# Kernel tuning notes

Measured on AMD Instinct MI355X. Metric: run time of the kernel, lower is better.

The kernel has to match this reference:

```python
import jax, jax.numpy as jnp
import numpy as np

D_MODEL = 1024
N_HEAD = 16
D_K = 64
D_V = 64
D_INNER = 4096
MAX_REL = 16
EPS = 1e-6


def _rel_index(length_q, length_k):
    # Shaw-style clipped relative distance matrix -> indices into embedding table
    dist = jnp.arange(length_k)[None, :] - jnp.arange(length_q)[:, None]
    return jnp.clip(dist, -MAX_REL, MAX_REL) + MAX_REL  # [Lq, Lk] in [0, 2*MAX_REL]


def _layer_norm(x, gamma, beta):
    mu = jnp.mean(x, axis=-1, keepdims=True)
    var = jnp.var(x, axis=-1, keepdims=True)
    return (x - mu) / jnp.sqrt(var + EPS) * gamma + beta


def setup_inputs() -> dict:
    key = jax.random.key(0)
    ks = jax.random.split(key, 16)
    B, L = 8, 1024
    s = 0.02
    inp = {
        "q": jax.random.normal(ks[0], (B, L, D_MODEL), jnp.float32),
        "k": jax.random.normal(ks[1], (B, L, D_MODEL), jnp.float32),
        "v": jax.random.normal(ks[2], (B, L, D_MODEL), jnp.float32),
        "wq": jax.random.normal(ks[3], (D_MODEL, D_MODEL), jnp.float32) * s,
        "bq": jnp.zeros((D_MODEL,), jnp.float32),
        "wk": jax.random.normal(ks[4], (D_MODEL, D_MODEL), jnp.float32) * s,
        "bk": jnp.zeros((D_MODEL,), jnp.float32),
        "wv": jax.random.normal(ks[5], (D_MODEL, D_MODEL), jnp.float32) * s,
        "bv": jnp.zeros((D_MODEL,), jnp.float32),
        "wfc": jax.random.normal(ks[6], (D_MODEL, D_MODEL), jnp.float32) * s,
        "bfc": jnp.zeros((D_MODEL,), jnp.float32),
        "w1": jax.random.normal(ks[7], (D_MODEL, D_INNER), jnp.float32) * s,
        "b1": jnp.zeros((D_INNER,), jnp.float32),
        "w2": jax.random.normal(ks[8], (D_INNER, D_MODEL), jnp.float32) * s,
        "b2": jnp.zeros((D_MODEL,), jnp.float32),
        "ln_g": jnp.ones((D_MODEL,), jnp.float32),
        "ln_b": jnp.zeros((D_MODEL,), jnp.float32),
        "rel_k": jax.random.normal(ks[9], (2 * MAX_REL + 1, D_K), jnp.float32) * s,
        "rel_v": jax.random.normal(ks[10], (2 * MAX_REL + 1, D_V), jnp.float32) * s,
    }
    return inp


def reference(q, k, v, wq, bq, wk, bk, wv, bv, wfc, bfc, w1, b1, w2, b2, ln_g, ln_b, rel_k, rel_v):
    B, Lq, _ = q.shape
    Lk = k.shape[1]
    residual = q

    Q = q @ wq + bq  # [B, Lq, D]
    K = k @ wk + bk
    V = v @ wv + bv

    Qh = Q.reshape(B, Lq, N_HEAD, D_K)  # [B, Lq, H, dk]
    Kh = K.reshape(B, Lk, N_HEAD, D_K)
    Vh = V.reshape(B, Lk, N_HEAD, D_V)

    # content-content scores
    attn1 = jnp.einsum("bqhd,bkhd->bhqk", Qh, Kh)
    # content-position scores (Shaw relative position)
    idx = _rel_index(Lq, Lk)  # [Lq, Lk]
    k2 = rel_k[idx]           # [Lq, Lk, dk]
    attn2 = jnp.einsum("bqhd,qkd->bhqk", Qh, k2)

    attn = (attn1 + attn2) / jnp.sqrt(jnp.float32(D_K))
    attn = jax.nn.softmax(attn, axis=-1)  # dropout = identity (eval)

    weight1 = jnp.einsum("bhqk,bkhd->bhqd", attn, Vh)
    v2 = rel_v[idx]  # [Lq, Lk, dv]
    weight2 = jnp.einsum("bhqk,qkd->bhqd", attn, v2)

    out = (weight1 + weight2).transpose(0, 2, 1, 3).reshape(B, Lq, N_HEAD * D_V)
    out = out @ wfc + bfc
    out = out + residual
    out = _layer_norm(out, ln_g, ln_b)

    residual = out
    out2 = jax.nn.relu(out @ w1 + b1) @ w2 + b2
    out = _layer_norm(out2 + residual, ln_g, ln_b)  # same LN params reused, as in source
    return out
```

## Files before the change

kernel.cpp:

```cpp
#include <hip/hip_runtime.h>
#include <stdint.h>


typedef __bf16 bf16x8 __attribute__((ext_vector_type(8)));
typedef float  f32x4  __attribute__((ext_vector_type(4)));

__device__ __forceinline__ unsigned short f2bf(float f) {
  __bf16 h = (__bf16)f;
  union { __bf16 h; unsigned short u; } x; x.h = h;
  return x.u;
}

__device__ __forceinline__ void gload_lds16(
    const unsigned short* g,
    __attribute__((address_space(3))) unsigned int* l) {
  __builtin_amdgcn_global_load_lds(
      (const __attribute__((address_space(1))) unsigned int*)g, l, 16, 0, 0);
}

template<int EPI>
__global__ __launch_bounds__(512, 2) void gemm_bt(
    const unsigned short* __restrict__ A,
    const unsigned short* __restrict__ Bt,
    const float* __restrict__ bias0,
    const float* __restrict__ bias1,
    const float* __restrict__ bias2,
    void* __restrict__ Cout,
    int M, int N, int K,
    size_t sA, size_t sB, size_t sC)
{
  __shared__ __align__(16) unsigned short S[3 * 24576];
  const int tid = threadIdx.x;
  const int lane = tid & 63, wv = tid >> 6;
  const int lq = lane >> 4, lm = lane & 15;
  const int wr = wv >> 2, wc = wv & 3;

  const int z = blockIdx.z;
  const float* bias = (z == 0) ? bias0 : (z == 1) ? bias1 : bias2;
  A  += (size_t)z * sA;
  Bt += (size_t)z * sB;

  const int nx = gridDim.x;
  const int nwg = nx * gridDim.y;
  int bid = blockIdx.y * nx + blockIdx.x;
  bid = (bid & 7) * (nwg >> 3) + (bid >> 3);
  const int m0 = (bid / nx) * 256, n0 = (bid % nx) * 128;

  const int srow = tid >> 3;
  const int scol = ((tid & 7) ^ (srow & 7)) * 8;
  const unsigned short* ga = A  + (size_t)(m0 + srow) * K + scol;
  const unsigned short* gb = Bt + (size_t)(n0 + srow) * K + scol;

  __attribute__((address_space(3))) unsigned int* lbase =
      (__attribute__((address_space(3))) unsigned int*)S;

  f32x4 acc[8][2] = {};

  auto stage = [&](int buf) {
    __attribute__((address_space(3))) unsigned int* lA = lbase + buf * 12288 + wv * 256;
    __attribute__((address_space(3))) unsigned int* lB = lA + 8192;
    #pragma unroll
    for (int g = 0; g < 4; ++g)
      gload_lds16(ga + (size_t)(g * 64) * K, lA + g * 2048);
    #pragma unroll
    for (int g = 0; g < 2; ++g)
      gload_lds16(gb + (size_t)(g * 64) * K, lB + g * 2048);
    ga += 64; gb += 64;
  };

  const int csw0 = ((lq ^ (lm & 7)) << 4);
  const int csw1 = csw0 ^ 64;
  const char* fa = (const char*)S + (wr * 128 + lm) * 128;
  const char* fb = (const char*)S + 32768 + (wc * 32 + lm) * 128;

  auto compute_tile = [&](int buf) {
    const char* ba = fa + buf * 49152;
    const char* bb = fb + buf * 49152;
    bf16x8 bfr[2][2];
    #pragma unroll
    for (int j = 0; j < 2; ++j) {
      bfr[j][0] = *(const bf16x8*)(bb + j * 2048 + csw0);
      bfr[j][1] = *(const bf16x8*)(bb + j * 2048 + csw1);
    }
    #pragma unroll
    for (int q = 0; q < 4; ++q) {
      bf16x8 af[2][2];
      #pragma unroll
      for (int ii = 0; ii < 2; ++ii) {
        af[ii][0] = *(const bf16x8*)(ba + (q * 2 + ii) * 2048 + csw0);
        af[ii][1] = *(const bf16x8*)(ba + (q * 2 + ii) * 2048 + csw1);
      }
      __builtin_amdgcn_s_barrier();
      __builtin_amdgcn_s_setprio(1);
      #pragma unroll
      for (int ii = 0; ii < 2; ++ii)
        #pragma unroll
        for (int j = 0; j < 2; ++j)
          #pragma unroll
          for (int kk = 0; kk < 2; ++kk)
            acc[q * 2 + ii][j] = __builtin_amdgcn_mfma_f32_16x16x32_bf16(
                af[ii][kk], bfr[j][kk], acc[q * 2 + ii][j], 0, 0, 0);
      __builtin_amdgcn_s_setprio(0);
      __builtin_amdgcn_s_barrier();
    }
  };

  const int nt = K >> 6;
  stage(0);
  stage(1);
  for (int t = 0; t < nt; ++t) {
    if (t + 1 < nt) asm volatile("s_waitcnt vmcnt(6)" ::: "memory");
    else            asm volatile("s_waitcnt vmcnt(0)" ::: "memory");
    __builtin_amdgcn_s_barrier();
    __builtin_amdgcn_sched_barrier(0);
    if (t + 2 < nt) stage((t + 2) % 3);
    compute_tile(t % 3);
  }

  #pragma unroll
  for (int i = 0; i < 8; ++i) {
    #pragma unroll
    for (int j = 0; j < 2; ++j) {
      const int col = n0 + wc * 32 + j * 16 + lm;
      const float bv = bias[col];
      #pragma unroll
      for (int r = 0; r < 4; ++r) {
        const int row = m0 + wr * 128 + i * 16 + lq * 4 + r;
        float v = acc[i][j][r] + bv;
        if (EPI == 2) v = fmaxf(v, 0.0f);
        if (EPI == 1) ((float*)Cout)[(size_t)row * N + col] = v;
        else ((unsigned short*)Cout + (size_t)z * sC)[(size_t)row * N + col] = f2bf(v);
      }
    }
  }
}

__global__ __launch_bounds__(256) void tcast(
    const float* __restrict__ in, unsigned short* __restrict__ out, int R, int C)
{
  __shared__ float tile[32][33];
  const int tx = threadIdx.x & 31, ty = threadIdx.x >> 5;
  const int r0 = blockIdx.y * 32, c0 = blockIdx.x * 32;
  #pragma unroll
  for (int s = 0; s < 4; ++s)
    tile[ty + s * 8][tx] = in[(size_t)(r0 + ty + s * 8) * C + c0 + tx];
  __syncthreads();
  #pragma unroll
  for (int s = 0; s < 4; ++s)
    out[(size_t)(c0 + ty + s * 8) * R + r0 + tx] = f2bf(tile[tx][ty + s * 8]);
}

__global__ __launch_bounds__(256) void cast4(
    const float* __restrict__ in, unsigned short* __restrict__ out, int n)
{
  int i = (blockIdx.x * 256 + threadIdx.x) * 4;
  if (i < n) {
    float4 v = *(const float4*)(in + i);
    ushort4 o;
    o.x = f2bf(v.x); o.y = f2bf(v.y); o.z = f2bf(v.z); o.w = f2bf(v.w);
    *(ushort4*)(out + i) = o;
  }
}

__global__ __launch_bounds__(256) void vtrans(
    const unsigned short* __restrict__ VP, unsigned short* __restrict__ VPT)
{
  __shared__ unsigned short tile[64 * 66];
  const int pt = blockIdx.x, h = blockIdx.y, b = blockIdx.z;
  const int tid = threadIdx.x;
  const int p = tid >> 2, c0 = (tid & 3) * 16;
  const unsigned short* src = VP + (size_t)(b * 1024 + pt * 64 + p) * 1024 + h * 64 + c0;
  union { uint4 q; unsigned int u[4]; } t0, t1;
  t0.q = *(const uint4*)src;
  t1.q = *(const uint4*)(src + 8);
  #pragma unroll
  for (int e = 0; e < 4; ++e) {
    *(unsigned int*)&tile[p * 66 + c0 + e * 2]     = t0.u[e];
    *(unsigned int*)&tile[p * 66 + c0 + 8 + e * 2] = t1.u[e];
  }
  __syncthreads();
  const int d = tid >> 2, p0 = (tid & 3) * 16;
  union { uint4 q[2]; unsigned short s[16]; } ob;
  #pragma unroll
  for (int e = 0; e < 16; ++e) ob.s[e] = tile[(p0 + e) * 66 + d];
  unsigned short* dst = VPT + ((size_t)(h * 64 + d) * 8 + b) * 1024 + pt * 64 + p0;
  *(uint4*)dst       = ob.q[0];
  *(uint4*)(dst + 8) = ob.q[1];
}

__global__ __launch_bounds__(256, 3) void attn_flash(
    const unsigned short* __restrict__ Qp,
    const unsigned short* __restrict__ Kp,
    const unsigned short* __restrict__ VPT,
    const float* __restrict__ relk,
    const float* __restrict__ relv,
    unsigned short* __restrict__ ctx)
{
  int id = (blockIdx.z * gridDim.y + blockIdx.y) * gridDim.x + blockIdx.x;
  id = (id & 7) * 256 + (id >> 3);
  const int qt = id & 15, h = (id >> 4) & 15, b = id >> 8;

  const int tid = threadIdx.x;
  const int lane = tid & 63, wv = tid >> 6;
  const int lq = lane >> 4, lm = lane & 15;

  __shared__ __align__(16) unsigned short Kt[64][72];
  __shared__ __align__(16) unsigned short Vt[64][72];
  __shared__ __align__(16) unsigned short Pt[64][72];
  __shared__ __align__(16) unsigned short relvT[64][32];
  __shared__ float qrel_s[64][33];
  __shared__ float Racc[64][33];

  const float CE = 0.125f * 1.44269504088896340736f;

  const int tok0 = b * 1024 + qt * 64;

  for (int i = tid; i < 64 * 33; i += 256) {
    const int rr = i / 33, ss = i - rr * 33;
    Racc[rr][ss] = 0.0f;
  }
  for (int i = tid; i < 64 * 32; i += 256) {
    const int dd = i >> 5, ss = i & 31;
    relvT[dd][ss] = f2bf(relv[ss * 64 + dd]);
  }

  bf16x8 qf0, qf1;
  {
    const unsigned short* qg = Qp + (size_t)(tok0 + wv * 16 + lm) * 1024 + h * 64;
    qf0 = *(const bf16x8*)(qg + lq * 8);
    qf1 = *(const bf16x8*)(qg + 32 + lq * 8);
  }

  #pragma unroll
  for (int t = 0; t < 3; ++t) {
    const int bin = t * 16 + lm;
    union { bf16x8 v; unsigned short s[8]; } rk0, rk1;
    #pragma unroll
    for (int e = 0; e < 8; ++e) { rk0.s[e] = 0; rk1.s[e] = 0; }
    if (bin < 33) {
      const float* rp = relk + bin * 64 + lq * 8;
      #pragma unroll
      for (int e = 0; e < 8; ++e) {
        rk0.s[e] = f2bf(rp[e]);
        rk1.s[e] = f2bf(rp[32 + e]);
      }
    }
    f32x4 Sr = {};
    Sr = __builtin_amdgcn_mfma_f32_16x16x32_bf16(qf0, rk0.v, Sr, 0, 0, 0);
    Sr = __builtin_amdgcn_mfma_f32_16x16x32_bf16(qf1, rk1.v, Sr, 0, 0, 0);
    if (bin < 33) {
      #pragma unroll
      for (int r = 0; r < 4; ++r) qrel_s[wv * 16 + lq * 4 + r][bin] = Sr[r] * CE;
    }
  }
  __syncthreads();

  float q0a[4], q32a[4];
  #pragma unroll
  for (int r = 0; r < 4; ++r) {
    const int rowl = wv * 16 + lq * 4 + r;
    q0a[r]  = qrel_s[rowl][0];
    q32a[r] = qrel_s[rowl][32];
  }

  union { bf16x8 v; unsigned short s[8]; } one8;
  #pragma unroll
  for (int e = 0; e < 8; ++e) one8.s[e] = 0x3F80;

  f32x4 Oa[4] = {};
  f32x4 Rs = {};
  float r0a[4] = {0, 0, 0, 0}, r32a[4] = {0, 0, 0, 0};

  const int srow = tid >> 2, scol = (tid & 3) * 16;
  const unsigned short* kg = Kp + (size_t)(b * 1024 + srow) * 1024 + h * 64 + scol;
  const unsigned short* vg = VPT + ((size_t)(h * 64 + srow) * 8 + b) * 1024 + scol;
  const int qa0 = qt * 64 + wv * 16;

  const int pread = wv * 16 + ((lm & 3) << 2) + (lm >> 2);

  uint4 rk0_ = *(const uint4*)(kg);
  uint4 rk1_ = *(const uint4*)(kg + 8);
  uint4 rv0_ = *(const uint4*)(vg);
  uint4 rv1_ = *(const uint4*)(vg + 8);

  for (int kt = 0; kt < 16; ++kt) {
    __syncthreads();
    *(uint4*)&Kt[srow][scol]     = rk0_;
    *(uint4*)&Kt[srow][scol + 8] = rk1_;
    *(uint4*)&Vt[srow][scol]     = rv0_;
    *(uint4*)&Vt[srow][scol + 8] = rv1_;
    if (kt < 15) {
      kg += 64 * 1024;
      vg += 64;
      rk0_ = *(const uint4*)(kg);
      rk1_ = *(const uint4*)(kg + 8);
      rv0_ = *(const uint4*)(vg);
      rv1_ = *(const uint4*)(vg + 8);
    }
    __syncthreads();

    #pragma unroll
    for (int tj = 0; tj < 4; ++tj) {
      bf16x8 kf0 = *(const bf16x8*)(&Kt[tj * 16 + lm][lq * 8]);
      bf16x8 kf1 = *(const bf16x8*)(&Kt[tj * 16 + lm][32 + lq * 8]);
      f32x4 S = {};
      S = __builtin_amdgcn_mfma_f32_16x16x32_bf16(qf0, kf0, S, 0, 0, 0);
      S = __builtin_amdgcn_mfma_f32_16x16x32_bf16(qf1, kf1, S, 0, 0, 0);
      const int c0 = kt * 64 + tj * 16;
      const int prow0 = wv * 16 + lq;
      if (c0 + 31 <= qa0) {
        #pragma unroll
        for (int r = 0; r < 4; ++r) {
          const float p = __builtin_amdgcn_exp2f(fmaf(S[r], CE, q0a[r]));
          r0a[r] += p;
          Pt[prow0 + r * 4][tj * 16 + lm] = f2bf(p);
        }
      } else if (c0 >= qa0 + 31) {
        #pragma unroll
        for (int r = 0; r < 4; ++r) {
          const float p = __builtin_amdgcn_exp2f(fmaf(S[r], CE, q32a[r]));
          r32a[r] += p;
          Pt[prow0 + r * 4][tj * 16 + lm] = f2bf(p);
        }
      } else {
        const int kpos = c0 + lm;
        #pragma unroll
        for (int r = 0; r < 4; ++r) {
          const int rowl = wv * 16 + lq * 4 + r;
          const int dist = kpos - (qt * 64 + rowl);
          const int bin = (dist < -16 ? 0 : (dist > 16 ? 32 : dist + 16));
          const float p = __builtin_amdgcn_exp2f(fmaf(S[r], CE, qrel_s[rowl][bin]));
          if (bin == 0)       r0a[r]  += p;
          else if (bin == 32) r32a[r] += p;
          else Racc[rowl][bin] = p;
          Pt[prow0 + r * 4][tj * 16 + lm] = f2bf(p);
        }
      }
    }
    bf16x8 pf0 = *(const bf16x8*)(&Pt[pread][lq * 8]);
    bf16x8 pf1 = *(const bf16x8*)(&Pt[pread][32 + lq * 8]);
    Rs = __builtin_amdgcn_mfma_f32_16x16x32_bf16(pf0, one8.v, Rs, 0, 0, 0);
    Rs = __builtin_amdgcn_mfma_f32_16x16x32_bf16(pf1, one8.v, Rs, 0, 0, 0);
    #pragma unroll
    for (int dt = 0; dt < 4; ++dt) {
      bf16x8 vf0 = *(const bf16x8*)(&Vt[dt * 16 + lm][lq * 8]);
      bf16x8 vf1 = *(const bf16x8*)(&Vt[dt * 16 + lm][32 + lq * 8]);
      Oa[dt] = __builtin_amdgcn_mfma_f32_16x16x32_bf16(pf0, vf0, Oa[dt], 0, 0, 0);
      Oa[dt] = __builtin_amdgcn_mfma_f32_16x16x32_bf16(pf1, vf1, Oa[dt], 0, 0, 0);
    }
  }

  #pragma unroll
  for (int r = 0; r < 4; ++r) {
    #pragma unroll
    for (int off = 1; off < 16; off <<= 1) {
      r0a[r]  += __shfl_xor(r0a[r],  off, 64);
      r32a[r] += __shfl_xor(r32a[r], off, 64);
    }
  }
  if (lm == 0) {
    #pragma unroll
    for (int r = 0; r < 4; ++r) Racc[wv * 16 + lq * 4 + r][0] = r0a[r];
  }
  __syncthreads();
  for (int i = tid; i < 64 * 32; i += 256) {
    const int rr = i >> 5, cc = i & 31;
    Pt[rr][cc] = f2bf(Racc[rr][cc]);
  }
  __syncthreads();

  bf16x8 raf = *(const bf16x8*)(&Pt[wv * 16 + lm][lq * 8]);
  #pragma unroll
  for (int dt = 0; dt < 4; ++dt) {
    bf16x8 rvb = *(const bf16x8*)(&relvT[dt * 16 + lm][lq * 8]);
    f32x4 O2 = {};
    O2 = __builtin_amdgcn_mfma_f32_16x16x32_bf16(raf, rvb, O2, 0, 0, 0);
    const float rv32 = relv[32 * 64 + dt * 16 + lm];
    #pragma unroll
    for (int r = 0; r < 4; ++r) {
      const int rowl = wv * 16 + lq * 4 + r;
      const float v = (Oa[dt][r] + O2[r] + r32a[r] * rv32) / Rs[r];
      ctx[(size_t)(tok0 + rowl) * 1024 + h * 64 + dt * 16 + lm] = f2bf(v);
    }
  }
}

template<bool WB>
__global__ __launch_bounds__(256) void ln_res(
    const float* __restrict__ x, const float* __restrict__ res,
    const float* __restrict__ g, const float* __restrict__ bta,
    float* __restrict__ of, unsigned short* __restrict__ ob)
{
  const int row = blockIdx.x;
  const int tid = threadIdx.x;
  __shared__ float red[8];
  const size_t base = (size_t)row * 1024 + tid * 4;
  const float4 xv = *(const float4*)(x + base);
  const float4 rv = *(const float4*)(res + base);
  float v0 = xv.x + rv.x, v1 = xv.y + rv.y, v2 = xv.z + rv.z, v3 = xv.w + rv.w;
  float s1 = v0 + v1 + v2 + v3;
  float s2 = v0 * v0 + v1 * v1 + v2 * v2 + v3 * v3;
  #pragma unroll
  for (int off = 1; off < 64; off <<= 1) {
    s1 += __shfl_xor(s1, off, 64);
    s2 += __shfl_xor(s2, off, 64);
  }
  const int wv = tid >> 6;
  if ((tid & 63) == 0) { red[wv * 2] = s1; red[wv * 2 + 1] = s2; }
  __syncthreads();
  s1 = red[0] + red[2] + red[4] + red[6];
  s2 = red[1] + red[3] + red[5] + red[7];
  const float mean = s1 * (1.f / 1024.f);
  const float var = s2 * (1.f / 1024.f) - mean * mean;
  const float rstd = rsqrtf(var + 1e-6f);
  const float4 gv = *(const float4*)(g + tid * 4);
  const float4 bv = *(const float4*)(bta + tid * 4);
  float y0 = (v0 - mean) * rstd * gv.x + bv.x;
  float y1 = (v1 - mean) * rstd * gv.y + bv.y;
  float y2 = (v2 - mean) * rstd * gv.z + bv.z;
  float y3 = (v3 - mean) * rstd * gv.w + bv.w;
  float4 yo; yo.x = y0; yo.y = y1; yo.z = y2; yo.w = y3;
  *(float4*)(of + base) = yo;
  if (WB) {
    ushort4 o;
    o.x = f2bf(y0); o.y = f2bf(y1); o.z = f2bf(y2); o.w = f2bf(y3);
    *(ushort4*)(ob + base) = o;
  }
}

extern "C" void kernel_launch(void* const* d_in, const int* in_sizes, int n_in,
                              void* d_out, int out_size, void* d_ws, size_t ws_size,
                              hipStream_t stream) {
  (void)in_sizes; (void)n_in; (void)out_size; (void)ws_size;
  const float* q    = (const float*)d_in[0];
  const float* k    = (const float*)d_in[1];
  const float* v    = (const float*)d_in[2];
  const float* wq   = (const float*)d_in[3];
  const float* bq   = (const float*)d_in[4];
  const float* wk   = (const float*)d_in[5];
  const float* bk   = (const float*)d_in[6];
  const float* wv_  = (const float*)d_in[7];
  const float* bv   = (const float*)d_in[8];
  const float* wfc  = (const float*)d_in[9];
  const float* bfc  = (const float*)d_in[10];
  const float* w1   = (const float*)d_in[11];
  const float* b1   = (const float*)d_in[12];
  const float* w2   = (const float*)d_in[13];
  const float* b2   = (const float*)d_in[14];
  const float* ln_g = (const float*)d_in[15];
  const float* ln_b = (const float*)d_in[16];
  const float* rel_k = (const float*)d_in[17];
  const float* rel_v = (const float*)d_in[18];

  char* ws = (char*)d_ws;
  const size_t MB = 1ull << 20;
  unsigned short* WQT  = (unsigned short*)(ws + 0 * MB);
  unsigned short* WKT  = (unsigned short*)(ws + 2 * MB);
  unsigned short* WVT  = (unsigned short*)(ws + 4 * MB);
  unsigned short* WFCT = (unsigned short*)(ws + 6 * MB);
  unsigned short* W1T  = (unsigned short*)(ws + 8 * MB);
  unsigned short* W2T  = (unsigned short*)(ws + 16 * MB);
  unsigned short* QP   = (unsigned short*)(ws + 24 * MB);
  unsigned short* KP   = (unsigned short*)(ws + 40 * MB);
  unsigned short* VP   = (unsigned short*)(ws + 56 * MB);
  unsigned short* QBF  = (unsigned short*)(ws + 72 * MB);
  unsigned short* KBF  = (unsigned short*)(ws + 88 * MB);
  unsigned short* VBF  = (unsigned short*)(ws + 104 * MB);
  unsigned short* VPT  = QBF;
  unsigned short* CTX  = KBF;
  float*          OTMP = (float*)(ws + 104 * MB);
  float*          X1F  = (float*)(ws + 24 * MB);
  unsigned short* X1BF = VP;
  unsigned short* HBUF = (unsigned short*)(ws + 72 * MB);
  float*          Y2   = (float*)(ws + 136 * MB);

  const dim3 blk(256);
  const dim3 gblk(512);
  const int NTOK = 8192;

  tcast<<<dim3(32, 32), blk, 0, stream>>>(wq, WQT, 1024, 1024);
  tcast<<<dim3(32, 32), blk, 0, stream>>>(wk, WKT, 1024, 1024);
  tcast<<<dim3(32, 32), blk, 0, stream>>>(wv_, WVT, 1024, 1024);
  tcast<<<dim3(32, 32), blk, 0, stream>>>(wfc, WFCT, 1024, 1024);
  tcast<<<dim3(128, 32), blk, 0, stream>>>(w1, W1T, 1024, 4096);
  tcast<<<dim3(32, 128), blk, 0, stream>>>(w2, W2T, 4096, 1024);
  cast4<<<8192, blk, 0, stream>>>(q, QBF, NTOK * 1024);
  cast4<<<8192, blk, 0, stream>>>(k, KBF, NTOK * 1024);
  cast4<<<8192, blk, 0, stream>>>(v, VBF, NTOK * 1024);

  gemm_bt<0><<<dim3(8, 32, 3), gblk, 0, stream>>>(
      QBF, WQT, bq, bk, bv, QP, NTOK, 1024, 1024,
      (size_t)8 * MB, (size_t)1 * MB, (size_t)8 * MB);

  vtrans<<<dim3(16, 16, 8), blk, 0, stream>>>(VP, VPT);

  attn_flash<<<dim3(16, 16, 8), blk, 0, stream>>>(QP, KP, VPT, rel_k, rel_v, CTX);

  gemm_bt<1><<<dim3(8, 32), gblk, 0, stream>>>(CTX, WFCT, bfc, bfc, bfc, OTMP,
                                               NTOK, 1024, 1024, 0, 0, 0);
  ln_res<true><<<8192, blk, 0, stream>>>(OTMP, q, ln_g, ln_b, X1F, X1BF);
  gemm_bt<2><<<dim3(32, 32), gblk, 0, stream>>>(X1BF, W1T, b1, b1, b1, HBUF,
                                                NTOK, 4096, 1024, 0, 0, 0);
  gemm_bt<1><<<dim3(8, 32), gblk, 0, stream>>>(HBUF, W2T, b2, b2, b2, Y2,
                                               NTOK, 1024, 4096, 0, 0, 0);
  ln_res<false><<<8192, blk, 0, stream>>>(Y2, X1F, ln_g, ln_b, (float*)d_out, nullptr);
}
```

Before: 607.5 us.

## Shrink attention LDS footprint with bf16 scratch and aliasing to raise occupancy

The relative-position score table and the relative-probability accumulator are now stored in bf16 instead of fp32. The rel_v transpose buffer now reuses the K tile region after the main loop, and all shared arrays are packed into a single pool. This cuts LDS per block so the launch bound can go from 3 to 4 blocks per CU, aiming to hide latency better. The P tile layout was also simplified to direct row stores. The costs are lower precision in the relative logits, a tighter register budget that may cause spills, and possibly different bank-conflict behaviour.

```diff
diff --git a/kernel.cpp b/kernel.cpp
--- a/kernel.cpp
+++ b/kernel.cpp
@@ -9,6 +9,9 @@
   __bf16 h = (__bf16)f;
   union { __bf16 h; unsigned short u; } x; x.h = h;
   return x.u;
+}
+__device__ __forceinline__ float bf2f(unsigned short h) {
+  union { unsigned u; float f; } x; x.u = ((unsigned)h) << 16; return x.f;
 }
 
 __device__ __forceinline__ void gload_lds16(
@@ -188,7 +191,7 @@
   *(uint4*)(dst + 8) = ob.q[1];
 }
 
-__global__ __launch_bounds__(256, 3) void attn_flash(
+__global__ __launch_bounds__(256, 4) void attn_flash(
     const unsigned short* __restrict__ Qp,
     const unsigned short* __restrict__ Kp,
     const unsigned short* __restrict__ VPT,
@@ -204,25 +207,19 @@
   const int lane = tid & 63, wv = tid >> 6;
   const int lq = lane >> 4, lm = lane & 15;
 
-  __shared__ __align__(16) unsigned short Kt[64][72];
-  __shared__ __align__(16) unsigned short Vt[64][72];
-  __shared__ __align__(16) unsigned short Pt[64][72];
-  __shared__ __align__(16) unsigned short relvT[64][32];
-  __shared__ float qrel_s[64][33];
-  __shared__ float Racc[64][33];
+  __shared__ __align__(16) unsigned short SM[18560];
+  unsigned short* Kt    = SM;
+  unsigned short* Vt    = SM + 4608;
+  unsigned short* Pt    = SM + 9216;
+  unsigned short* RaccB = SM + 13824;
+  unsigned short* qrelB = SM + 16384;
+  unsigned short* relvT = SM;
 
   const float CE = 0.125f * 1.44269504088896340736f;
 
   const int tok0 = b * 1024 + qt * 64;
 
-  for (int i = tid; i < 64 * 33; i += 256) {
-    const int rr = i / 33, ss = i - rr * 33;
-    Racc[rr][ss] = 0.0f;
-  }
-  for (int i = tid; i < 64 * 32; i += 256) {
-    const int dd = i >> 5, ss = i & 31;
-    relvT[dd][ss] = f2bf(relv[ss * 64 + dd]);
-  }
+  for (int i = tid; i < 64 * 40; i += 256) RaccB[i] = 0;
 
   bf16x8 qf0, qf1;
   {
@@ -250,7 +247,8 @@
     Sr = __builtin_amdgcn_mfma_f32_16x16x32_bf16(qf1, rk1.v, Sr, 0, 0, 0);
     if (bin < 33) {
       #pragma unroll
-      for (int r = 0; r < 4; ++r) qrel_s[wv * 16 + lq * 4 + r][bin] = Sr[r] * CE;
+      for (int r = 0; r < 4; ++r)
+        qrelB[(wv * 16 + lq * 4 + r) * 34 + bin] = f2bf(Sr[r] * CE);
     }
   }
   __syncthreads();
@@ -259,8 +257,8 @@
   #pragma unroll
   for (int r = 0; r < 4; ++r) {
     const int rowl = wv * 16 + lq * 4 + r;
-    q0a[r]  = qrel_s[rowl][0];
-    q32a[r] = qrel_s[rowl][32];
+    q0a[r]  = bf2f(qrelB[rowl * 34 + 0]);
+    q32a[r] = bf2f(qrelB[rowl * 34 + 32]);
   }
 
   union { bf16x8 v; unsigned short s[8]; } one8;
@@ -276,8 +274,6 @@
   const unsigned short* vg = VPT + ((size_t)(h * 64 + srow) * 8 + b) * 1024 + scol;
   const int qa0 = qt * 64 + wv * 16;
 
-  const int pread = wv * 16 + ((lm & 3) << 2) + (lm >> 2);
-
   uint4 rk0_ = *(const uint4*)(kg);
   uint4 rk1_ = *(const uint4*)(kg + 8);
   uint4 rv0_ = *(const uint4*)(vg);
@@ -285,10 +281,10 @@
 
   for (int kt = 0; kt < 16; ++kt) {
     __syncthreads();
-    *(uint4*)&Kt[srow][scol]     = rk0_;
-    *(uint4*)&Kt[srow][scol + 8] = rk1_;
-    *(uint4*)&Vt[srow][scol]     = rv0_;
-    *(uint4*)&Vt[srow][scol + 8] = rv1_;
+    *(uint4*)(Kt + srow * 72 + scol)     = rk0_;
+    *(uint4*)(Kt + srow * 72 + scol + 8) = rk1_;
+    *(uint4*)(Vt + srow * 72 + scol)     = rv0_;
+    *(uint4*)(Vt + srow * 72 + scol + 8) = rv1_;
     if (kt < 15) {
       kg += 64 * 1024;
       vg += 64;
@@ -301,26 +297,25 @@
 
     #pragma unroll
     for (int tj = 0; tj < 4; ++tj) {
-      bf16x8 kf0 = *(const bf16x8*)(&Kt[tj * 16 + lm][lq * 8]);
-      bf16x8 kf1 = *(const bf16x8*)(&Kt[tj * 16 + lm][32 + lq * 8]);
+      bf16x8 kf0 = *(const bf16x8*)(Kt + (tj * 16 + lm) * 72 + lq * 8);
+      bf16x8 kf1 = *(const bf16x8*)(Kt + (tj * 16 + lm) * 72 + 32 + lq * 8);
       f32x4 S = {};
       S = __builtin_amdgcn_mfma_f32_16x16x32_bf16(qf0, kf0, S, 0, 0, 0);
       S = __builtin_amdgcn_mfma_f32_16x16x32_bf16(qf1, kf1, S, 0, 0, 0);
       const int c0 = kt * 64 + tj * 16;
-      const int prow0 = wv * 16 + lq;
       if (c0 + 31 <= qa0) {
         #pragma unroll
         for (int r = 0; r < 4; ++r) {
           const float p = __builtin_amdgcn_exp2f(fmaf(S[r], CE, q0a[r]));
           r0a[r] += p;
-          Pt[prow0 + r * 4][tj * 16 + lm] = f2bf(p);
+          Pt[(wv * 16 + lq * 4 + r) * 72 + tj * 16 + lm] = f2bf(p);
         }
       } else if (c0 >= qa0 + 31) {
         #pragma unroll
         for (int r = 0; r < 4; ++r) {
           const float p = __builtin_amdgcn_exp2f(fmaf(S[r], CE, q32a[r]));
           r32a[r] += p;
-          Pt[prow0 + r * 4][tj * 16 + lm] = f2bf(p);
+          Pt[(wv * 16 + lq * 4 + r) * 72 + tj * 16 + lm] = f2bf(p);
         }
       } else {
         const int kpos = c0 + lm;
@@ -329,22 +324,23 @@
           const int rowl = wv * 16 + lq * 4 + r;
           const int dist = kpos - (qt * 64 + rowl);
           const int bin = (dist < -16 ? 0 : (dist > 16 ? 32 : dist + 16));
-          const float p = __builtin_amdgcn_exp2f(fmaf(S[r], CE, qrel_s[rowl][bin]));
+          const float p =
+              __builtin_amdgcn_exp2f(fmaf(S[r], CE, bf2f(qrelB[rowl * 34 + bin])));
           if (bin == 0)       r0a[r]  += p;
           else if (bin == 32) r32a[r] += p;
-          else Racc[rowl][bin] = p;
-          Pt[prow0 + r * 4][tj * 16 + lm] = f2bf(p);
+          else RaccB[rowl * 40 + bin] = f2bf(p);
+          Pt[rowl * 72 + tj * 16 + lm] = f2bf(p);
         }
       }
     }
-    bf16x8 pf0 = *(const bf16x8*)(&Pt[pread][lq * 8]);
-    bf16x8 pf1 = *(const bf16x8*)(&Pt[pread][32 + lq * 8]);
+    bf16x8 pf0 = *(const bf16x8*)(Pt + (wv * 16 + lm) * 72 + lq * 8);
+    bf16x8 pf1 = *(const bf16x8*)(Pt + (wv * 16 + lm) * 72 + 32 + lq * 8);
     Rs = __builtin_amdgcn_mfma_f32_16x16x32_bf16(pf0, one8.v, Rs, 0, 0, 0);
     Rs = __builtin_amdgcn_mfma_f32_16x16x32_bf16(pf1, one8.v, Rs, 0, 0, 0);
     #pragma unroll
     for (int dt = 0; dt < 4; ++dt) {
-      bf16x8 vf0 = *(const bf16x8*)(&Vt[dt * 16 + lm][lq * 8]);
-      bf16x8 vf1 = *(const bf16x8*)(&Vt[dt * 16 + lm][32 + lq * 8]);
+      bf16x8 vf0 = *(const bf16x8*)(Vt + (dt * 16 + lm) * 72 + lq * 8);
+      bf16x8 vf1 = *(const bf16x8*)(Vt + (dt * 16 + lm) * 72 + 32 + lq * 8);
       Oa[dt] = __builtin_amdgcn_mfma_f32_16x16x32_bf16(pf0, vf0, Oa[dt], 0, 0, 0);
       Oa[dt] = __builtin_amdgcn_mfma_f32_16x16x32_bf16(pf1, vf1, Oa[dt], 0, 0, 0);
     }
@@ -360,19 +356,20 @@
   }
   if (lm == 0) {
     #pragma unroll
-    for (int r = 0; r < 4; ++r) Racc[wv * 16 + lq * 4 + r][0] = r0a[r];
+    for (int r = 0; r < 4; ++r)
+      RaccB[(wv * 16 + lq * 4 + r) * 40 + 0] = f2bf(r0a[r]);
   }
   __syncthreads();
   for (int i = tid; i < 64 * 32; i += 256) {
-    const int rr = i >> 5, cc = i & 31;
-    Pt[rr][cc] = f2bf(Racc[rr][cc]);
+    const int dd = i >> 5, ss = i & 31;
+    relvT[dd * 32 + ss] = f2bf(relv[ss * 64 + dd]);
   }
   __syncthreads();
 
-  bf16x8 raf = *(const bf16x8*)(&Pt[wv * 16 + lm][lq * 8]);
+  bf16x8 raf = *(const bf16x8*)(RaccB + (wv * 16 + lm) * 40 + lq * 8);
   #pragma unroll
   for (int dt = 0; dt < 4; ++dt) {
-    bf16x8 rvb = *(const bf16x8*)(&relvT[dt * 16 + lm][lq * 8]);
+    bf16x8 rvb = *(const bf16x8*)(relvT + (dt * 16 + lm) * 32 + lq * 8);
     f32x4 O2 = {};
     O2 = __builtin_amdgcn_mfma_f32_16x16x32_bf16(raf, rvb, O2, 0, 0, 0);
     const float rv32 = relv[32 * 64 + dt * 16 + lm];
```

New measurement: 608.0 us. Within noise of the previous version (+0.1%).
